# Kernel optimization log

Measured on AMD Instinct MI355X. Metric: run time of the kernel, lower is better.

Reference implementation:

```python
import jax, jax.numpy as jnp
import numpy as np

N_U, N_I, E = 100000, 200000, 500000
CH, H, HD, L, OUT, B_SEED = 128, 4, 32, 2, 64, 1024
NEG_SLOPE = 0.2
LN_EPS = 1e-5


def setup_inputs() -> dict:
    key = jax.random.key(0)
    ks = jax.random.split(key, 24)
    s = 1.0 / np.sqrt(CH)
    inp = {
        'x_user': jax.random.normal(ks[0], (N_U, CH), jnp.float32),
        'x_item': jax.random.normal(ks[1], (N_I, CH), jnp.float32),
        'ui_src': jax.random.randint(ks[2], (E,), 0, N_U, jnp.int32),
        'ui_dst': jax.random.randint(ks[3], (E,), 0, N_I, jnp.int32),
        'iu_src': jax.random.randint(ks[4], (E,), 0, N_I, jnp.int32),
        'iu_dst': jax.random.randint(ks[5], (E,), 0, N_U, jnp.int32),
        'Wsrc_ui': jax.random.normal(ks[6], (L, CH, CH), jnp.float32) * s,
        'Wdst_ui': jax.random.normal(ks[7], (L, CH, CH), jnp.float32) * s,
        'asrc_ui': jax.random.normal(ks[8], (L, H, HD), jnp.float32) * s,
        'adst_ui': jax.random.normal(ks[9], (L, H, HD), jnp.float32) * s,
        'b_ui': jnp.zeros((L, CH), jnp.float32),
        'Wsrc_iu': jax.random.normal(ks[10], (L, CH, CH), jnp.float32) * s,
        'Wdst_iu': jax.random.normal(ks[11], (L, CH, CH), jnp.float32) * s,
        'asrc_iu': jax.random.normal(ks[12], (L, H, HD), jnp.float32) * s,
        'adst_iu': jax.random.normal(ks[13], (L, H, HD), jnp.float32) * s,
        'b_iu': jnp.zeros((L, CH), jnp.float32),
        'ln_w_user': jnp.ones((L, CH), jnp.float32),
        'ln_b_user': jnp.zeros((L, CH), jnp.float32),
        'ln_w_item': jnp.ones((L, CH), jnp.float32),
        'ln_b_item': jnp.zeros((L, CH), jnp.float32),
        'lin_w': jax.random.normal(ks[14], (CH, OUT), jnp.float32) * s,
        'lin_b': jnp.zeros((OUT,), jnp.float32),
        'B': B_SEED,
    }
    return inp


def _gat_conv(x_src, x_dst, src, dst, Ws, Wd, a_s, a_d, b):
    # Bipartite GATConv (PyG semantics, add_self_loops=False, concat=True).
    n_dst = x_dst.shape[0]
    hs = (x_src @ Ws).reshape(-1, H, HD)   # [Ns,H,HD]
    hd = (x_dst @ Wd).reshape(-1, H, HD)   # [Nd,H,HD]
    es = jnp.einsum('nhc,hc->nh', hs, a_s)  # per-node src logits
    ed = jnp.einsum('nhc,hc->nh', hd, a_d)  # per-node dst logits
    e = jax.nn.leaky_relu(es[src] + ed[dst], NEG_SLOPE)  # [E,H]
    # segment softmax over incoming edges of each dst node
    m = jax.ops.segment_max(e, dst, num_segments=n_dst)
    w = jnp.exp(e - m[dst])
    z = jax.ops.segment_sum(w, dst, num_segments=n_dst)
    alpha = w / (z[dst] + 1e-16)
    out = jax.ops.segment_sum(hs[src] * alpha[:, :, None], dst, num_segments=n_dst)
    return out.reshape(n_dst, H * HD) + b


def _layer_norm(x, w, b):
    mu = jnp.mean(x, axis=-1, keepdims=True)
    var = jnp.var(x, axis=-1, keepdims=True)
    return (x - mu) * jax.lax.rsqrt(var + LN_EPS) * w + b


def reference(x_user, x_item, ui_src, ui_dst, iu_src, iu_dst,
              Wsrc_ui, Wdst_ui, asrc_ui, adst_ui, b_ui,
              Wsrc_iu, Wdst_iu, asrc_iu, adst_iu, b_iu,
              ln_w_user, ln_b_user, ln_w_item, ln_b_item,
              lin_w, lin_b, B):
    for l in range(L):
        # HeteroConv with edge_aggr='sum'; each dst node type receives from one edge type here
        xu = _gat_conv(x_item, x_user, iu_src, iu_dst,
                       Wsrc_iu[l], Wdst_iu[l], asrc_iu[l], adst_iu[l], b_iu[l])
        xi = _gat_conv(x_user, x_item, ui_src, ui_dst,
                       Wsrc_ui[l], Wdst_ui[l], asrc_ui[l], adst_ui[l], b_ui[l])
        x_user = jax.nn.relu(_layer_norm(xu, ln_w_user[l], ln_b_user[l]))
        x_item = jax.nn.relu(_layer_norm(xi, ln_w_item[l], ln_b_item[l]))
    return x_user[:B] @ lin_w + lin_b
```

## Files before the change

### kernel.cpp

```cpp
#include <hip/hip_runtime.h>

#define CH 128
#define NHEAD 4
#define CAP 16

typedef float f32x4 __attribute__((ext_vector_type(4)));
typedef short bf16x8 __attribute__((ext_vector_type(8)));

static __device__ __forceinline__ float b2f(unsigned short u){
  union { unsigned int u; float f; } x; x.u = ((unsigned int)u) << 16; return x.f;
}
static __device__ __forceinline__ unsigned short f2b(float f){
  union { float f; unsigned int u; } x; x.f = f;
  unsigned int r = x.u + 0x7FFFu + ((x.u >> 16) & 1u);
  return (unsigned short)(r >> 16);
}

static __host__ __device__ inline int cdiv_i(int a, int b){ return (a + b - 1) / b; }

__global__ __launch_bounds__(256) void hg_bscat(
    const int* __restrict__ dstU, const int* __restrict__ srcU,
    int* __restrict__ cntU, int* __restrict__ slotsU,
    int* __restrict__ spNU, int* __restrict__ spDU, int* __restrict__ spSU,
    const int* __restrict__ dstI, const int* __restrict__ srcI,
    int* __restrict__ cntI, int* __restrict__ slotsI,
    int* __restrict__ spNI, int* __restrict__ spDI, int* __restrict__ spSI,
    int E, int half){
  int b = blockIdx.x;
  const int *dst, *src; int *cnt, *slots, *spN, *spD, *spS; int lb;
  if (b < half){ dst=dstU; src=srcU; cnt=cntU; slots=slotsU; spN=spNU; spD=spDU; spS=spSU; lb=b; }
  else { dst=dstI; src=srcI; cnt=cntI; slots=slotsI; spN=spNI; spD=spDI; spS=spSI; lb=b-half; }
  int t = lb*256 + threadIdx.x;
  if (t >= E) return;
  int d = dst[t], s = src[t];
  int pos = atomicAdd(&cnt[d], 1);
  if (pos < CAP){
    slots[(size_t)d*CAP + pos] = s;
  } else {
    int sp = atomicAdd(spN, 1);
    spD[sp] = d; spS[sp] = s;
  }
}

__global__ __launch_bounds__(256) void hg_prep1(
    const float* __restrict__ xu, unsigned short* __restrict__ yu, long nuv, long nut, int bu,
    const float* __restrict__ xi, unsigned short* __restrict__ yi, long niv, long nit, int bi,
    const float* __restrict__ Wsrc_iu, const float* __restrict__ Wsrc_ui,
    const float* __restrict__ Wdst_iu, const float* __restrict__ Wdst_ui,
    const float* __restrict__ asrc_iu, const float* __restrict__ asrc_ui,
    const float* __restrict__ adst_iu, const float* __restrict__ adst_ui,
    unsigned short* __restrict__ wtAll, float* __restrict__ wdAll, float* __restrict__ wsAll){
  int b = blockIdx.x, tid = threadIdx.x;
  if (b < bu + bi){
    const float* x; unsigned short* y; long nv, nt; int lb;
    if (b < bu){ x = xu; y = yu; nv = nuv; nt = nut; lb = b; }
    else { x = xi; y = yi; nv = niv; nt = nit; lb = b - bu; }
    long t = ((long)lb * 256 + tid) * 4;
    if (t >= nt) return;
    ushort4 o;
    if (t + 3 < nv){
      float4 v = *(const float4*)(x + t);
      o.x = f2b(v.x); o.y = f2b(v.y); o.z = f2b(v.z); o.w = f2b(v.w);
    } else {
      o.x = o.y = o.z = o.w = 0;
    }
    *(ushort4*)(y + t) = o;
  } else {
    int wb = b - bu - bi;
    int ld = wb / 68, r = wb % 68;
    int l = ld >> 1, d = ld & 1;
    const float* Ws = (d ? Wsrc_ui : Wsrc_iu) + (size_t)l*CH*CH;
    const float* Wd = (d ? Wdst_ui : Wdst_iu) + (size_t)l*CH*CH;
    const float* as_ = (d ? asrc_ui : asrc_iu) + (size_t)l*CH;
    const float* ad  = (d ? adst_ui : adst_iu) + (size_t)l*CH;
    unsigned short* wt = wtAll + (size_t)ld*CH*CH;
    float* wd_o = wdAll + (size_t)ld*CH*4;
    float* ws_o = wsAll + (size_t)ld*CH*4;
    if (r < 64){
      int t = r*256 + tid;
      int k = t >> 7, n = t & 127;
      wt[n*CH + k] = f2b(Ws[t]);
    } else if (r < 66){
      int t = (r - 64)*256 + tid;
      int k = t >> 2, h = t & 3;
      float acc = 0.f;
      #pragma unroll 8
      for (int c = 0; c < 32; ++c) acc += Wd[k*CH + h*32 + c] * ad[h*32 + c];
      wd_o[k*4 + h] = acc;
    } else {
      int t = (r - 66)*256 + tid;
      int k = t >> 2, h = t & 3;
      float acc = 0.f;
      #pragma unroll 8
      for (int c = 0; c < 32; ++c) acc += Ws[k*CH + h*32 + c] * as_[h*32 + c];
      ws_o[k*4 + h] = acc;
    }
  }
}

__global__ __launch_bounds__(256) void hg_gemm2(const unsigned short* __restrict__ X0,
                                                const unsigned short* __restrict__ W0,
                                                unsigned short* __restrict__ Y0, int n0,
                                                const unsigned short* __restrict__ X1,
                                                const unsigned short* __restrict__ W1,
                                                unsigned short* __restrict__ Y1, int n01,
                                                const float* __restrict__ wsU, const float* __restrict__ wdU,
                                                float* __restrict__ esU, float* __restrict__ edU, int NU, int bU,
                                                const float* __restrict__ wsI, const float* __restrict__ wdI,
                                                float* __restrict__ esI, float* __restrict__ edI, int NI){
  __shared__ unsigned short Abuf[CH*CH];
  __shared__ unsigned short Bbuf[CH*CH];
  int tid = threadIdx.x;
  int b = blockIdx.x;

  if (b >= n01){
    int eb = b - n01;
    const unsigned short* x; const float *wsf, *wdf; float *es, *ed; int N, lb;
    if (eb < bU){ x = X1; wsf = wsU; wdf = wdU; es = esU; ed = edU; N = NU; lb = eb; }
    else { x = X0; wsf = wsI; wdf = wdI; es = esI; ed = edI; N = NI; lb = eb - bU; }
    int n = lb * 256 + tid;
    if (n >= N) return;
    const uint4* row = (const uint4*)(x + (size_t)n * CH);
    float s0=0.f,s1=0.f,s2=0.f,s3=0.f,d0=0.f,d1=0.f,d2=0.f,d3=0.f;
    #pragma unroll
    for (int b8 = 0; b8 < 16; ++b8){
      uint4 v = row[b8];
      unsigned int u[4] = {v.x, v.y, v.z, v.w};
      #pragma unroll
      for (int q = 0; q < 4; ++q){
        int k = b8*8 + 2*q;
        float x0 = b2f((unsigned short)(u[q] & 0xffffu));
        float x1 = b2f((unsigned short)(u[q] >> 16));
        float4 a0 = *(const float4*)(wsf + (size_t)k*4);
        float4 a1 = *(const float4*)(wsf + (size_t)(k+1)*4);
        float4 c0 = *(const float4*)(wdf + (size_t)k*4);
        float4 c1 = *(const float4*)(wdf + (size_t)(k+1)*4);
        s0 += x0*a0.x + x1*a1.x;  s1 += x0*a0.y + x1*a1.y;
        s2 += x0*a0.z + x1*a1.z;  s3 += x0*a0.w + x1*a1.w;
        d0 += x0*c0.x + x1*c1.x;  d1 += x0*c0.y + x1*c1.y;
        d2 += x0*c0.z + x1*c1.z;  d3 += x0*c0.w + x1*c1.w;
      }
    }
    float* eo = es + (size_t)n*4;
    eo[0]=s0; eo[1]=s1; eo[2]=s2; eo[3]=s3;
    float* do_ = ed + (size_t)n*4;
    do_[0]=d0; do_[1]=d1; do_[2]=d2; do_[3]=d3;
    return;
  }

  size_t bm = b;
  const unsigned short* X; const unsigned short* W; unsigned short* Y;
  if ((int)bm < n0){ X = X0; W = W0; Y = Y0; }
  else { X = X1; W = W1; Y = Y1; bm -= n0; }
  const unsigned short* xsrc = X + bm * (size_t)(CH*CH);
  #pragma unroll
  for (int it = 0; it < 8; ++it){
    int G = it*256 + tid;
    int m = G >> 4, kg = G & 15;
    int sw = kg ^ (m & 7);
    uint4 va = ((const uint4*)xsrc)[G];
    ((uint4*)Abuf)[m*16 + sw] = va;
    uint4 vb = ((const uint4*)W)[G];
    ((uint4*)Bbuf)[m*16 + sw] = vb;
  }
  __syncthreads();

  int lane = tid & 63, wid = tid >> 6;
  int wr = wid >> 1, wc = wid & 1;
  int l15 = lane & 15, l4 = lane >> 4;
  f32x4 acc[4][4] = {};

  #pragma unroll
  for (int kk = 0; kk < 4; ++kk){
    int kgq = kk*4 + l4;
    bf16x8 af[4], bfr[4];
    #pragma unroll
    for (int i = 0; i < 4; ++i){
      int r = wr*64 + i*16 + l15;
      af[i] = *(const bf16x8*)&Abuf[(r*16 + (kgq ^ (r & 7))) * 8];
      int c = wc*64 + i*16 + l15;
      bfr[i] = *(const bf16x8*)&Bbuf[(c*16 + (kgq ^ (c & 7))) * 8];
    }
    #pragma unroll
    for (int i = 0; i < 4; ++i)
      #pragma unroll
      for (int j = 0; j < 4; ++j)
        acc[i][j] = __builtin_amdgcn_mfma_f32_16x16x32_bf16(af[i], bfr[j], acc[i][j], 0, 0, 0);
  }

  #pragma unroll
  for (int i = 0; i < 4; ++i){
    #pragma unroll
    for (int j = 0; j < 4; ++j){
      int r0 = wr*64 + i*16 + l4*4;
      int c  = wc*64 + j*16 + l15;
      size_t base = (bm*CH + r0) * (size_t)CH + c;
      #pragma unroll
      for (int v = 0; v < 4; ++v)
        Y[base + (size_t)v*CH] = f2b(acc[i][j][v]);
    }
  }
}

#define AGG_ROUND(DEPTH)                                                          \
  for (int j0 = 0; j0 < nb16; j0 += DEPTH){                                       \
    uint4 hv[DEPTH]; float lg[DEPTH];                                             \
    _Pragma("unroll")                                                             \
    for (int k = 0; k < DEPTH; ++k){                                              \
      int jk = j0 + k; jk = (jk < nb16) ? jk : (nb16 - 1);                        \
      int s = __shfl(sj, g*16 + jk);                                              \
      hv[k] = *(const uint4*)(hs + (size_t)s*CH + c16*8);                         \
      lg[k] = eslog[(size_t)s*4 + h];                                             \
    }                                                                             \
    _Pragma("unroll")                                                             \
    for (int k = 0; k < DEPTH; ++k){                                              \
      float ev = lg[k] + edv;                                                     \
      ev = (ev > 0.f) ? ev : 0.2f * ev;                                           \
      float w = ((j0 + k) < nb16) ? __expf(ev) : 0.f;                             \
      zp += w;                                                                    \
      unsigned int u0 = hv[k].x, u1 = hv[k].y, u2 = hv[k].z, u3 = hv[k].w;        \
      pacc[0] += w * b2f((unsigned short)(u0 & 0xffffu));                         \
      pacc[1] += w * b2f((unsigned short)(u0 >> 16));                             \
      pacc[2] += w * b2f((unsigned short)(u1 & 0xffffu));                         \
      pacc[3] += w * b2f((unsigned short)(u1 >> 16));                             \
      pacc[4] += w * b2f((unsigned short)(u2 & 0xffffu));                         \
      pacc[5] += w * b2f((unsigned short)(u2 >> 16));                             \
      pacc[6] += w * b2f((unsigned short)(u3 & 0xffffu));                         \
      pacc[7] += w * b2f((unsigned short)(u3 >> 16));                             \
    }                                                                             \
  }

__global__ __launch_bounds__(256) void hg_agg2(
    const int* __restrict__ cntU, const int* __restrict__ slotsU,
    const int* __restrict__ spNU, const int* __restrict__ spDU, const int* __restrict__ spSU,
    const float* __restrict__ eslogU, const float* __restrict__ edU,
    const unsigned short* __restrict__ hsI,
    const float* __restrict__ biasU, const float* __restrict__ lnwU, const float* __restrict__ lnbU,
    unsigned short* __restrict__ xoutU, int NU, int nbU,
    const int* __restrict__ cntI, const int* __restrict__ slotsI,
    const int* __restrict__ spNI, const int* __restrict__ spDI, const int* __restrict__ spSI,
    const float* __restrict__ eslogI, const float* __restrict__ edI,
    const unsigned short* __restrict__ hsU,
    const float* __restrict__ biasI, const float* __restrict__ lnwI, const float* __restrict__ lnbI,
    unsigned short* __restrict__ xoutI, int NI){
  int b = blockIdx.x;
  bool isU = (b < nbU);
  const int *cnt, *slots, *spN, *spD, *spS; const float *eslog, *ed;
  const unsigned short* hs; const float *bias, *lnw, *lnb;
  unsigned short* xout; int Ndst, lb;
  if (isU){
    cnt = cntU; slots = slotsU; spN = spNU; spD = spDU; spS = spSU;
    eslog = eslogU; ed = edU; hs = hsI;
    bias = biasU; lnw = lnwU; lnb = lnbU; xout = xoutU; Ndst = NU; lb = b;
  } else {
    cnt = cntI; slots = slotsI; spN = spNI; spD = spDI; spS = spSI;
    eslog = eslogI; ed = edI; hs = hsU;
    bias = biasI; lnw = lnwI; lnb = lnbI; xout = xoutI; Ndst = NI; lb = b - nbU;
  }
  int tid = threadIdx.x;
  int lane = tid & 63, wid = tid >> 6;
  int g = lane >> 4, c16 = lane & 15, h = c16 >> 2;
  int node = lb * 16 + wid * 4 + g;
  uint4* orow = (uint4*)(xout + (size_t)node * CH);
  if (node >= Ndst){
    uint4 z4 = {0,0,0,0};
    orow[c16] = z4;
    return;
  }

  int deg = cnt[node];
  float edv = ed[(size_t)node*4 + h];
  float pacc[8] = {0.f,0.f,0.f,0.f,0.f,0.f,0.f,0.f};
  float zp = 0.f;

  int nb16 = deg < CAP ? deg : CAP;
  const int* sl = slots + (size_t)node * CAP;
  int jj = (c16 < nb16) ? c16 : (nb16 > 0 ? nb16 - 1 : 0);
  int sj = sl[jj];

  if (isU){
    AGG_ROUND(8)
  } else {
    AGG_ROUND(4)
  }
  if (deg > CAP){
    int sn = *spN;
    for (int j = 0; j < sn; ++j){
      if (spD[j] == node){
        int s = spS[j];
        float ev = eslog[(size_t)s*4 + h] + edv;
        ev = (ev > 0.f) ? ev : 0.2f * ev;
        float w = __expf(ev);
        zp += w;
        uint4 hv1 = *(const uint4*)(hs + (size_t)s*CH + c16*8);
        unsigned int u[4] = {hv1.x, hv1.y, hv1.z, hv1.w};
        #pragma unroll
        for (int q = 0; q < 4; ++q){
          pacc[2*q]   += w * b2f((unsigned short)(u[q] & 0xffffu));
          pacc[2*q+1] += w * b2f((unsigned short)(u[q] >> 16));
        }
      }
    }
  }

  float rz = (zp > 0.f) ? (1.f / zp) : 0.f;
  float4 b0 = *(const float4*)(bias + c16*8);
  float4 b1 = *(const float4*)(bias + c16*8 + 4);
  float r[8];
  r[0] = pacc[0]*rz + b0.x; r[1] = pacc[1]*rz + b0.y;
  r[2] = pacc[2]*rz + b0.z; r[3] = pacc[3]*rz + b0.w;
  r[4] = pacc[4]*rz + b1.x; r[5] = pacc[5]*rz + b1.y;
  r[6] = pacc[6]*rz + b1.z; r[7] = pacc[7]*rz + b1.w;

  float s1 = 0.f, s2 = 0.f;
  #pragma unroll
  for (int k = 0; k < 8; ++k){ s1 += r[k]; s2 += r[k]*r[k]; }
  #pragma unroll
  for (int off = 1; off < 16; off <<= 1){
    s1 += __shfl_xor(s1, off);
    s2 += __shfl_xor(s2, off);
  }
  float mean = s1 * (1.f/128.f);
  float var  = s2 * (1.f/128.f) - mean*mean;
  float inv  = rsqrtf(var + 1e-5f);

  float4 w0 = *(const float4*)(lnw + c16*8);
  float4 w1 = *(const float4*)(lnw + c16*8 + 4);
  float4 l0 = *(const float4*)(lnb + c16*8);
  float4 l1 = *(const float4*)(lnb + c16*8 + 4);
  float y[8];
  y[0] = (r[0]-mean)*inv*w0.x + l0.x; y[1] = (r[1]-mean)*inv*w0.y + l0.y;
  y[2] = (r[2]-mean)*inv*w0.z + l0.z; y[3] = (r[3]-mean)*inv*w0.w + l0.w;
  y[4] = (r[4]-mean)*inv*w1.x + l1.x; y[5] = (r[5]-mean)*inv*w1.y + l1.y;
  y[6] = (r[6]-mean)*inv*w1.z + l1.z; y[7] = (r[7]-mean)*inv*w1.w + l1.w;
  uint4 o;
  unsigned int* op = (unsigned int*)&o;
  #pragma unroll
  for (int q = 0; q < 4; ++q){
    float a = fmaxf(y[2*q], 0.f), bb = fmaxf(y[2*q+1], 0.f);
    op[q] = (unsigned int)f2b(a) | ((unsigned int)f2b(bb) << 16);
  }
  orow[c16] = o;
}

__global__ __launch_bounds__(256) void hg_final(const unsigned short* __restrict__ x,
                                                const float* __restrict__ w,
                                                const float* __restrict__ b,
                                                float* __restrict__ out, int total, int OUTC){
  int t = blockIdx.x * 256 + threadIdx.x;
  if (t >= total) return;
  int r = t / OUTC, c = t % OUTC;
  const unsigned short* xr = x + (size_t)r * CH;
  float acc = b[c];
  #pragma unroll 8
  for (int k = 0; k < CH; ++k)
    acc += b2f(xr[k]) * w[(size_t)k * OUTC + c];
  out[t] = acc;
}

extern "C" void kernel_launch(void* const* d_in, const int* in_sizes, int n_in,
                              void* d_out, int out_size, void* d_ws, size_t ws_size,
                              hipStream_t stream){
  const float* x_user_f = (const float*)d_in[0];
  const float* x_item_f = (const float*)d_in[1];
  const int* ui_src = (const int*)d_in[2];
  const int* ui_dst = (const int*)d_in[3];
  const int* iu_src = (const int*)d_in[4];
  const int* iu_dst = (const int*)d_in[5];
  const float* Wsrc_ui = (const float*)d_in[6];
  const float* Wdst_ui = (const float*)d_in[7];
  const float* asrc_ui = (const float*)d_in[8];
  const float* adst_ui = (const float*)d_in[9];
  const float* b_ui    = (const float*)d_in[10];
  const float* Wsrc_iu = (const float*)d_in[11];
  const float* Wdst_iu = (const float*)d_in[12];
  const float* asrc_iu = (const float*)d_in[13];
  const float* adst_iu = (const float*)d_in[14];
  const float* b_iu    = (const float*)d_in[15];
  const float* ln_w_user = (const float*)d_in[16];
  const float* ln_b_user = (const float*)d_in[17];
  const float* ln_w_item = (const float*)d_in[18];
  const float* ln_b_item = (const float*)d_in[19];
  const float* lin_w = (const float*)d_in[20];
  const float* lin_b = (const float*)d_in[21];

  const int NU = in_sizes[0] / CH;
  const int NI = in_sizes[1] / CH;
  const int E  = in_sizes[2];
  const int Lnum = in_sizes[6] / (CH*CH);
  const int OUTC = in_sizes[21];
  const int Bn = out_size / OUTC;

  const int NUp = ((NU + 127) / 128) * 128;
  const int NIp = ((NI + 127) / 128) * 128;

  char* ws = (char*)d_ws;
  size_t off = 0;
  auto alloc = [&](size_t bytes)->char*{
    size_t r = (off + 255) & ~(size_t)255;
    off = r + bytes;
    return ws + r;
  };
  unsigned short* xu0 = (unsigned short*)alloc((size_t)NUp * CH * 2);
  unsigned short* xu1 = (unsigned short*)alloc((size_t)NUp * CH * 2);
  unsigned short* xi0 = (unsigned short*)alloc((size_t)NIp * CH * 2);
  unsigned short* xi1 = (unsigned short*)alloc((size_t)NIp * CH * 2);
  unsigned short* hsI = (unsigned short*)alloc((size_t)NIp * CH * 2);
  unsigned short* hsU = (unsigned short*)alloc((size_t)NUp * CH * 2);
  float* esIb = (float*)alloc((size_t)NIp * 4 * 4);
  float* esUb = (float*)alloc((size_t)NUp * 4 * 4);
  float* edU  = (float*)alloc((size_t)NUp * 4 * 4);
  float* edI  = (float*)alloc((size_t)NIp * 4 * 4);
  unsigned short* wtAll = (unsigned short*)alloc((size_t)Lnum * 2 * CH * CH * 2);
  float* wdAll = (float*)alloc((size_t)Lnum * 2 * CH * 4 * 4);
  float* wsAll = (float*)alloc((size_t)Lnum * 2 * CH * 4 * 4);
  int* cntAll = (int*)alloc((size_t)(NU + NI + 2) * 4);
  int* cnt_u = cntAll;
  int* cnt_i = cntAll + NU;
  int* spN_u = cntAll + NU + NI;
  int* spN_i = cntAll + NU + NI + 1;
  int* slots_u = (int*)alloc((size_t)NU * CAP * 4);
  int* slots_i = (int*)alloc((size_t)NI * CAP * 4);
  int* spD_u = (int*)alloc((size_t)E * 4);
  int* spS_u = (int*)alloc((size_t)E * 4);
  int* spD_i = (int*)alloc((size_t)E * 4);
  int* spS_i = (int*)alloc((size_t)E * 4);

  hipMemsetAsync(cntAll, 0, (size_t)(NU + NI + 2) * 4, stream);
  {
    int half = cdiv_i(E, 256);
    hg_bscat<<<dim3(2*half), dim3(256), 0, stream>>>(
        iu_dst, iu_src, cnt_u, slots_u, spN_u, spD_u, spS_u,
        ui_dst, ui_src, cnt_i, slots_i, spN_i, spD_i, spS_i, E, half);
  }
  {
    int bu = cdiv_i(NUp*CH/4, 256), bi = cdiv_i(NIp*CH/4, 256);
    int wp = Lnum*2*68;
    hg_prep1<<<dim3(bu + bi + wp), dim3(256), 0, stream>>>(
        x_user_f, xu0, (long)NU*CH, (long)NUp*CH, bu,
        x_item_f, xi0, (long)NI*CH, (long)NIp*CH, bi,
        Wsrc_iu, Wsrc_ui, Wdst_iu, Wdst_ui,
        asrc_iu, asrc_ui, adst_iu, adst_ui,
        wtAll, wdAll, wsAll);
  }

  unsigned short *xuA = xu0, *xuB = xu1, *xiA = xi0, *xiB = xi1;
  const int nbkI = NIp/128, nbkU = NUp/128;
  const int bU_esed = cdiv_i(NU, 256), bI_esed = cdiv_i(NI, 256);
  const int aggU = NUp/16, aggI = NIp/16;

  for (int l = 0; l < Lnum; ++l){
    size_t ao = (size_t)l * CH;
    const unsigned short* wtA = wtAll + (size_t)(l*2 + 0) * CH * CH;
    const unsigned short* wtB = wtAll + (size_t)(l*2 + 1) * CH * CH;
    const float* wdA = wdAll + (size_t)(l*2 + 0) * CH * 4;
    const float* wdB = wdAll + (size_t)(l*2 + 1) * CH * 4;
    const float* wsA = wsAll + (size_t)(l*2 + 0) * CH * 4;
    const float* wsB = wsAll + (size_t)(l*2 + 1) * CH * 4;

    hg_gemm2<<<dim3(nbkI + nbkU + bU_esed + bI_esed), dim3(256), 0, stream>>>(
        xiA, wtA, hsI, nbkI,
        xuA, wtB, hsU, nbkI + nbkU,
        wsB, wdA, esUb, edU, NU, bU_esed,
        wsA, wdB, esIb, edI, NI);
    hg_agg2<<<dim3(aggU + aggI), dim3(256), 0, stream>>>(
        cnt_u, slots_u, spN_u, spD_u, spS_u, esIb, edU, hsI,
        b_iu + ao, ln_w_user + ao, ln_b_user + ao, xuB, NU, aggU,
        cnt_i, slots_i, spN_i, spD_i, spS_i, esUb, edI, hsU,
        b_ui + ao, ln_w_item + ao, ln_b_item + ao, xiB, NI);

    unsigned short* t;
    t = xuA; xuA = xuB; xuB = t;
    t = xiA; xiA = xiB; xiB = t;
  }

  hg_final<<<dim3(cdiv_i(Bn*OUTC,256)), dim3(256), 0, stream>>>(xuA, lin_w, lin_b, (float*)d_out, Bn*OUTC, OUTC);
}
```

Before: 353.6 us.

## Fuse next-layer attention logit projections into aggregation epilogue

```diff
diff --git a/kernel.cpp b/kernel.cpp
--- a/kernel.cpp
+++ b/kernel.cpp
@@ -237,25 +237,33 @@
     const unsigned short* __restrict__ hsI,
     const float* __restrict__ biasU, const float* __restrict__ lnwU, const float* __restrict__ lnbU,
     unsigned short* __restrict__ xoutU, int NU, int nbU,
+    const float* __restrict__ wsNU, const float* __restrict__ wdNU,
+    float* __restrict__ esNU, float* __restrict__ edNU,
     const int* __restrict__ cntI, const int* __restrict__ slotsI,
     const int* __restrict__ spNI, const int* __restrict__ spDI, const int* __restrict__ spSI,
     const float* __restrict__ eslogI, const float* __restrict__ edI,
     const unsigned short* __restrict__ hsU,
     const float* __restrict__ biasI, const float* __restrict__ lnwI, const float* __restrict__ lnbI,
-    unsigned short* __restrict__ xoutI, int NI){
+    unsigned short* __restrict__ xoutI, int NI,
+    const float* __restrict__ wsNI, const float* __restrict__ wdNI,
+    float* __restrict__ esNI, float* __restrict__ edNI,
+    int fuse){
   int b = blockIdx.x;
   bool isU = (b < nbU);
   const int *cnt, *slots, *spN, *spD, *spS; const float *eslog, *ed;
   const unsigned short* hs; const float *bias, *lnw, *lnb;
+  const float *wsN, *wdN; float *esN, *edN;
   unsigned short* xout; int Ndst, lb;
   if (isU){
     cnt = cntU; slots = slotsU; spN = spNU; spD = spDU; spS = spSU;
     eslog = eslogU; ed = edU; hs = hsI;
     bias = biasU; lnw = lnwU; lnb = lnbU; xout = xoutU; Ndst = NU; lb = b;
+    wsN = wsNU; wdN = wdNU; esN = esNU; edN = edNU;
   } else {
     cnt = cntI; slots = slotsI; spN = spNI; spD = spDI; spS = spSI;
     eslog = eslogI; ed = edI; hs = hsU;
     bias = biasI; lnw = lnwI; lnb = lnbI; xout = xoutI; Ndst = NI; lb = b - nbU;
+    wsN = wsNI; wdN = wdNI; esN = esNI; edN = edNI;
   }
   int tid = threadIdx.x;
   int lane = tid & 63, wid = tid >> 6;
@@ -329,18 +337,38 @@
   float4 l0 = *(const float4*)(lnb + c16*8);
   float4 l1 = *(const float4*)(lnb + c16*8 + 4);
   float y[8];
-  y[0] = (r[0]-mean)*inv*w0.x + l0.x; y[1] = (r[1]-mean)*inv*w0.y + l0.y;
-  y[2] = (r[2]-mean)*inv*w0.z + l0.z; y[3] = (r[3]-mean)*inv*w0.w + l0.w;
-  y[4] = (r[4]-mean)*inv*w1.x + l1.x; y[5] = (r[5]-mean)*inv*w1.y + l1.y;
-  y[6] = (r[6]-mean)*inv*w1.z + l1.z; y[7] = (r[7]-mean)*inv*w1.w + l1.w;
+  y[0] = fmaxf((r[0]-mean)*inv*w0.x + l0.x, 0.f); y[1] = fmaxf((r[1]-mean)*inv*w0.y + l0.y, 0.f);
+  y[2] = fmaxf((r[2]-mean)*inv*w0.z + l0.z, 0.f); y[3] = fmaxf((r[3]-mean)*inv*w0.w + l0.w, 0.f);
+  y[4] = fmaxf((r[4]-mean)*inv*w1.x + l1.x, 0.f); y[5] = fmaxf((r[5]-mean)*inv*w1.y + l1.y, 0.f);
+  y[6] = fmaxf((r[6]-mean)*inv*w1.z + l1.z, 0.f); y[7] = fmaxf((r[7]-mean)*inv*w1.w + l1.w, 0.f);
   uint4 o;
   unsigned int* op = (unsigned int*)&o;
   #pragma unroll
-  for (int q = 0; q < 4; ++q){
-    float a = fmaxf(y[2*q], 0.f), bb = fmaxf(y[2*q+1], 0.f);
-    op[q] = (unsigned int)f2b(a) | ((unsigned int)f2b(bb) << 16);
-  }
+  for (int q = 0; q < 4; ++q)
+    op[q] = (unsigned int)f2b(y[2*q]) | ((unsigned int)f2b(y[2*q+1]) << 16);
   orow[c16] = o;
+
+  if (fuse){
+    float4 e4 = {0.f,0.f,0.f,0.f}, d4 = {0.f,0.f,0.f,0.f};
+    #pragma unroll
+    for (int j = 0; j < 8; ++j){
+      int c = c16*8 + j;
+      float yv = y[j];
+      float4 wsv = *(const float4*)(wsN + (size_t)c*4);
+      float4 wdv = *(const float4*)(wdN + (size_t)c*4);
+      e4.x += yv*wsv.x; e4.y += yv*wsv.y; e4.z += yv*wsv.z; e4.w += yv*wsv.w;
+      d4.x += yv*wdv.x; d4.y += yv*wdv.y; d4.z += yv*wdv.z; d4.w += yv*wdv.w;
+    }
+    #pragma unroll
+    for (int off = 1; off < 16; off <<= 1){
+      e4.x += __shfl_xor(e4.x, off); e4.y += __shfl_xor(e4.y, off);
+      e4.z += __shfl_xor(e4.z, off); e4.w += __shfl_xor(e4.w, off);
+      d4.x += __shfl_xor(d4.x, off); d4.y += __shfl_xor(d4.y, off);
+      d4.z += __shfl_xor(d4.z, off); d4.w += __shfl_xor(d4.w, off);
+    }
+    if (c16 == 0)      *(float4*)(esN + (size_t)node*4) = e4;
+    else if (c16 == 1) *(float4*)(edN + (size_t)node*4) = d4;
+  }
 }
 
 __global__ __launch_bounds__(256) void hg_final(const unsigned short* __restrict__ x,
@@ -407,10 +435,13 @@
   unsigned short* xi1 = (unsigned short*)alloc((size_t)NIp * CH * 2);
   unsigned short* hsI = (unsigned short*)alloc((size_t)NIp * CH * 2);
   unsigned short* hsU = (unsigned short*)alloc((size_t)NUp * CH * 2);
-  float* esIb = (float*)alloc((size_t)NIp * 4 * 4);
-  float* esUb = (float*)alloc((size_t)NUp * 4 * 4);
-  float* edU  = (float*)alloc((size_t)NUp * 4 * 4);
-  float* edI  = (float*)alloc((size_t)NIp * 4 * 4);
+  float* esI_[2]; float* esU_[2]; float* edU_[2]; float* edI_[2];
+  for (int p = 0; p < 2; ++p){
+    esI_[p] = (float*)alloc((size_t)NIp * 4 * 4);
+    esU_[p] = (float*)alloc((size_t)NUp * 4 * 4);
+    edU_[p] = (float*)alloc((size_t)NUp * 4 * 4);
+    edI_[p] = (float*)alloc((size_t)NIp * 4 * 4);
+  }
   unsigned short* wtAll = (unsigned short*)alloc((size_t)Lnum * 2 * CH * CH * 2);
   float* wdAll = (float*)alloc((size_t)Lnum * 2 * CH * 4 * 4);
   float* wsAll = (float*)alloc((size_t)Lnum * 2 * CH * 4 * 4);
@@ -451,6 +482,7 @@
 
   for (int l = 0; l < Lnum; ++l){
     size_t ao = (size_t)l * CH;
+    int rs = l & 1, wsx = rs ^ 1;
     const unsigned short* wtA = wtAll + (size_t)(l*2 + 0) * CH * CH;
     const unsigned short* wtB = wtAll + (size_t)(l*2 + 1) * CH * CH;
     const float* wdA = wdAll + (size_t)(l*2 + 0) * CH * 4;
@@ -458,16 +490,35 @@
     const float* wsA = wsAll + (size_t)(l*2 + 0) * CH * 4;
     const float* wsB = wsAll + (size_t)(l*2 + 1) * CH * 4;
 
-    hg_gemm2<<<dim3(nbkI + nbkU + bU_esed + bI_esed), dim3(256), 0, stream>>>(
-        xiA, wtA, hsI, nbkI,
-        xuA, wtB, hsU, nbkI + nbkU,
-        wsB, wdA, esUb, edU, NU, bU_esed,
-        wsA, wdB, esIb, edI, NI);
+    if (l == 0){
+      hg_gemm2<<<dim3(nbkI + nbkU + bU_esed + bI_esed), dim3(256), 0, stream>>>(
+          xiA, wtA, hsI, nbkI,
+          xuA, wtB, hsU, nbkI + nbkU,
+          wsB, wdA, esU_[rs], edU_[rs], NU, bU_esed,
+          wsA, wdB, esI_[rs], edI_[rs], NI);
+    } else {
+      hg_gemm2<<<dim3(nbkI + nbkU), dim3(256), 0, stream>>>(
+          xiA, wtA, hsI, nbkI,
+          xuA, wtB, hsU, nbkI + nbkU,
+          wsB, wdA, esU_[rs], edU_[rs], NU, 0,
+          wsA, wdB, esI_[rs], edI_[rs], NI);
+    }
+
+    int fuse = (l + 1 < Lnum) ? 1 : 0;
+    int ln = fuse ? (l + 1) : l;
+    const float* wsNA = wsAll + (size_t)(ln*2 + 0) * CH * 4;
+    const float* wsNB = wsAll + (size_t)(ln*2 + 1) * CH * 4;
+    const float* wdNA = wdAll + (size_t)(ln*2 + 0) * CH * 4;
+    const float* wdNB = wdAll + (size_t)(ln*2 + 1) * CH * 4;
+
     hg_agg2<<<dim3(aggU + aggI), dim3(256), 0, stream>>>(
-        cnt_u, slots_u, spN_u, spD_u, spS_u, esIb, edU, hsI,
+        cnt_u, slots_u, spN_u, spD_u, spS_u, esI_[rs], edU_[rs], hsI,
         b_iu + ao, ln_w_user + ao, ln_b_user + ao, xuB, NU, aggU,
-        cnt_i, slots_i, spN_i, spD_i, spS_i, esUb, edI, hsU,
-        b_ui + ao, ln_w_item + ao, ln_b_item + ao, xiB, NI);
+        wsNB, wdNA, esU_[wsx], edU_[wsx],
+        cnt_i, slots_i, spN_i, spD_i, spS_i, esU_[rs], edI_[rs], hsU,
+        b_ui + ao, ln_w_item + ao, ln_b_item + ao, xiB, NI,
+        wsNA, wdNB, esI_[wsx], edI_[wsx],
+        fuse);
 
     unsigned short* t;
     t = xuA; xuA = xuB; xuB = t;
```

Result: slower. 443.2 us (+25.3%).
